# Performance work log

Measured on AMD Instinct MI355X. Metric: run time of the kernel, lower is better.

## Reference

```python
import jax, jax.numpy as jnp
import numpy as np

MAX_LANES = 5
DELTA_V = 1.0
DELTA_D = 6.0


def setup_inputs() -> dict:
    key = jax.random.key(0)
    k1, k2 = jax.random.split(key)
    targets = jax.random.randint(k1, (32, 360, 640), 0, 6, dtype=jnp.int32)
    embedding_vector = jax.random.normal(k2, (32, 4, 360, 640), dtype=jnp.float32)
    return {"targets": targets, "embedding_vector": embedding_vector}


def reference(targets, embedding_vector):
    B, C, H, W = embedding_vector.shape
    L = MAX_LANES
    P = H * W
    t = targets.reshape(B, P)                      # [B,P] labels 0..L
    e = embedding_vector.reshape(B, C, P)          # [B,C,P]

    # per-(batch, lane) segment counts and means
    onehot = (t[:, None, :] == jnp.arange(1, L + 1, dtype=t.dtype)[None, :, None])  # [B,L,P]
    counts = onehot.sum(-1)                        # [B,L] int
    valid = counts > 1                             # lane used only if >1 points
    sums = jnp.einsum('blp,bcp->blc', onehot.astype(e.dtype), e)   # [B,L,C]
    means = sums / jnp.maximum(counts, 1)[..., None].astype(e.dtype)  # [B,L,C]

    # ---- variance (pull) loss: per-point distance to its lane mean ----
    means_ext = jnp.concatenate([jnp.zeros((B, 1, C), e.dtype), means], axis=1)  # [B,L+1,C]
    mean_pix = jnp.take_along_axis(means_ext, t[..., None].astype(jnp.int32), axis=1)  # [B,P,C]
    diff = e.transpose(0, 2, 1) - mean_pix         # [B,P,C]
    sq = jnp.sum(diff * diff, axis=-1)             # [B,P]
    dist = jnp.sqrt(jnp.maximum(sq, 1e-12))
    valid_ext = jnp.concatenate([jnp.zeros((B, 1), bool), valid], axis=1)  # [B,L+1]
    pix_valid = jnp.take_along_axis(valid_ext, t.astype(jnp.int32), axis=1)  # [B,P]
    hinge = jax.nn.relu(dist - DELTA_V)
    dist_sum = jnp.sum(jnp.where(pix_valid, hinge * hinge, 0.0))
    point_count = jnp.sum(jnp.where(valid, counts, 0)).astype(e.dtype)
    dist_loss = jnp.where(point_count > 0, dist_sum / jnp.maximum(point_count, 1.0), 0.0)

    # ---- distance (push) loss: pdist over valid lane means per batch ----
    d = means[:, :, None, :] - means[:, None, :, :]          # [B,L,L,C]
    psq = jnp.sum(d * d, axis=-1)                            # [B,L,L]
    pd = jnp.sqrt(jnp.maximum(psq, 1e-12))
    iu = jnp.arange(L)
    pair_mask = valid[:, :, None] & valid[:, None, :] & (iu[:, None] < iu[None, :])  # [B,L,L]
    ph = jax.nn.relu(DELTA_D - pd)
    per_batch_sum = jnp.sum(jnp.where(pair_mask, ph * ph, 0.0), axis=(1, 2))  # [B]
    npairs = pair_mask.sum((1, 2)).astype(e.dtype)           # [B]
    batch_has = npairs > 0                                   # needs >=2 valid lanes
    var_b = jnp.where(batch_has, per_batch_sum / jnp.maximum(npairs, 1.0), 0.0)
    n_batches = batch_has.sum().astype(e.dtype)
    var_loss = jnp.where(n_batches > 0, var_b.sum() / jnp.maximum(n_batches, 1.0), 0.0)

    return dist_loss + var_loss
```

## Files before the change

kernel.cpp:

```cpp
#include <hip/hip_runtime.h>
#include <math.h>

#define B 32
#define C 4
#define P (360*640)
#define L 5
#define DELTA_V 1.0f
#define DELTA_D 6.0f

#define BLKX 45
#define ITER1 5
#define NBLK3 (B*BLKX)
#define PSTRIDE 48

__device__ __forceinline__ float waveReduce(float v) {
#pragma unroll
    for (int off = 32; off; off >>= 1) v += __shfl_down(v, off, 64);
    return v;
}

__global__ __launch_bounds__(256, 4) void seg_sums_k(const int* __restrict__ tgt,
                                                     const float* __restrict__ emb,
                                                     float* __restrict__ partial,
                                                     unsigned char* __restrict__ tpk) {
    const int x = blockIdx.x, c = blockIdx.y, b = blockIdx.z;
    const int tid = threadIdx.x;

    const int4*   t4 = (const int4*)(tgt + (size_t)b * P);
    const float4* ec = (const float4*)(emb + ((size_t)b * C + c) * P);

    int4   tv[ITER1];
    float4 ev[ITER1];
#pragma unroll
    for (int it = 0; it < ITER1; ++it) {
        const int g = (x + it * BLKX) * 256 + tid;
        tv[it] = t4[g];
        ev[it] = ec[g];
    }

    if (c == 0) {
        uchar4* tp4 = (uchar4*)(tpk + (size_t)b * P);
#pragma unroll
        for (int it = 0; it < ITER1; ++it) {
            const int g = (x + it * BLKX) * 256 + tid;
            tp4[g] = make_uchar4((unsigned char)tv[it].x, (unsigned char)tv[it].y,
                                 (unsigned char)tv[it].z, (unsigned char)tv[it].w);
        }
    }

    float s[L], n[L];
#pragma unroll
    for (int l = 0; l < L; ++l) { s[l] = 0.f; n[l] = 0.f; }

    auto acc1 = [&](int tt, float e) {
#pragma unroll
        for (int l = 0; l < L; ++l) {
            float m = (tt == l + 1) ? 1.0f : 0.0f;
            n[l] += m;
            s[l] = fmaf(m, e, s[l]);
        }
    };
#pragma unroll
    for (int it = 0; it < ITER1; ++it) {
        acc1(tv[it].x, ev[it].x);
        acc1(tv[it].y, ev[it].y);
        acc1(tv[it].z, ev[it].z);
        acc1(tv[it].w, ev[it].w);
    }

    float vals[2*L];
#pragma unroll
    for (int l = 0; l < L; ++l) { vals[l] = s[l]; vals[L + l] = n[l]; }

    __shared__ float red[4][2*L];
    const int lane = tid & 63, wave = tid >> 6;
#pragma unroll
    for (int k = 0; k < 2*L; ++k) {
        float r = waveReduce(vals[k]);
        if (lane == 0) red[wave][k] = r;
    }
    __syncthreads();
    if (tid < L) {
        const float r = red[0][tid] + red[1][tid] + red[2][tid] + red[3][tid];
        partial[((size_t)b * 25 + c * L + tid) * PSTRIDE + x] = r;
    } else if (c == 0 && tid < 2*L) {
        const float r = red[0][tid] + red[1][tid] + red[2][tid] + red[3][tid];
        partial[((size_t)b * 25 + 20 + (tid - L)) * PSTRIDE + x] = r;
    }
}

__global__ __launch_bounds__(256, 4) void pull_k(const unsigned char* __restrict__ tpk,
                                                 const float* __restrict__ emb,
                                                 const float* __restrict__ partial,
                                                 float* __restrict__ meansG,
                                                 float* __restrict__ validG,
                                                 float* __restrict__ cntvG,
                                                 float* __restrict__ pullp) {
    __shared__ float  praw[25];
    __shared__ float4 lmean[L + 1];
    __shared__ float  lvalid[L + 1];
    __shared__ float  lred[4];
    const int xb = blockIdx.x, b = blockIdx.y;
    const int tid = threadIdx.x;
    const int lane = tid & 63, wave = tid >> 6;

    for (int v = wave; v < 25; v += 4) {
        float pv = (lane < BLKX) ? partial[((size_t)b * 25 + v) * PSTRIDE + lane] : 0.f;
        pv = waveReduce(pv);
        if (lane == 0) praw[v] = pv;
    }
    __syncthreads();
    if (tid < L) {
        const float cnt = praw[20 + tid];
        const bool  vld = cnt > 1.5f;
        const float inv = 1.0f / fmaxf(cnt, 1.0f);
        float4 m = make_float4(praw[tid] * inv, praw[5 + tid] * inv,
                               praw[10 + tid] * inv, praw[15 + tid] * inv);
        lmean[tid + 1]  = m;
        lvalid[tid + 1] = vld ? 1.f : 0.f;
        if (xb == 0) {
            *(float4*)(meansG + ((size_t)b * L + tid) * 4) = m;
            validG[b * L + tid] = vld ? 1.f : 0.f;
            cntvG[b * L + tid]  = vld ? cnt : 0.f;
        }
    }
    if (tid == 8) { lmean[0] = make_float4(0.f, 0.f, 0.f, 0.f); lvalid[0] = 0.f; }
    __syncthreads();

    const uchar4* tp4 = (const uchar4*)(tpk + (size_t)b * P);
    const float4* e0  = (const float4*)(emb + ((size_t)b * C + 0) * P);
    const float4* e1  = (const float4*)(emb + ((size_t)b * C + 1) * P);
    const float4* e2  = (const float4*)(emb + ((size_t)b * C + 2) * P);
    const float4* e3  = (const float4*)(emb + ((size_t)b * C + 3) * P);

    float acc = 0.f;
    auto proc1 = [&](int tt, float v0, float v1, float v2, float v3) {
        float4 m = lmean[tt];
        float d0 = v0 - m.x, d1 = v1 - m.y, d2 = v2 - m.z, d3 = v3 - m.w;
        float sq   = d0*d0 + d1*d1 + d2*d2 + d3*d3;
        float dist = sqrtf(fmaxf(sq, 1e-12f));
        float h    = fmaxf(dist - DELTA_V, 0.f);
        acc = fmaf(lvalid[tt] * h, h, acc);
    };
    auto consume = [&](uchar4 t, const float4& a0, const float4& a1,
                       const float4& a2, const float4& a3) {
        proc1(t.x, a0.x, a1.x, a2.x, a3.x);
        proc1(t.y, a0.y, a1.y, a2.y, a3.y);
        proc1(t.z, a0.z, a1.z, a2.z, a3.z);
        proc1(t.w, a0.w, a1.w, a2.w, a3.w);
    };

    {
        const int g0 = xb * 256 + tid, g1 = (xb + BLKX) * 256 + tid;
        uchar4 t0 = tp4[g0], t1 = tp4[g1];
        float4 a0 = e0[g0], a1 = e1[g0], a2 = e2[g0], a3 = e3[g0];
        float4 b0 = e0[g1], b1 = e1[g1], b2 = e2[g1], b3 = e3[g1];
        consume(t0, a0, a1, a2, a3);
        consume(t1, b0, b1, b2, b3);
    }
    {
        const int g0 = (xb + 2*BLKX) * 256 + tid, g1 = (xb + 3*BLKX) * 256 + tid;
        uchar4 t0 = tp4[g0], t1 = tp4[g1];
        float4 a0 = e0[g0], a1 = e1[g0], a2 = e2[g0], a3 = e3[g0];
        float4 b0 = e0[g1], b1 = e1[g1], b2 = e2[g1], b3 = e3[g1];
        consume(t0, a0, a1, a2, a3);
        consume(t1, b0, b1, b2, b3);
    }
    {
        const int g0 = (xb + 4*BLKX) * 256 + tid;
        uchar4 t0 = tp4[g0];
        float4 a0 = e0[g0], a1 = e1[g0], a2 = e2[g0], a3 = e3[g0];
        consume(t0, a0, a1, a2, a3);
    }

    float r = waveReduce(acc);
    if (lane == 0) lred[wave] = r;
    __syncthreads();
    if (tid == 0)
        pullp[b * BLKX + xb] = lred[0] + lred[1] + lred[2] + lred[3];
}

__global__ __launch_bounds__(256) void finish_k(const float* __restrict__ pullp,
                                                const float* __restrict__ meansG,
                                                const float* __restrict__ validG,
                                                const float* __restrict__ cntvG,
                                                float* __restrict__ out) {
    __shared__ float red[4][4];
    const int tid = threadIdx.x;
    const int lane = tid & 63, wave = tid >> 6;

    float vb = 0.f, has = 0.f;
    if (tid < B) {
        const float* mb = meansG + tid * L * 4;
        const float* vv = validG + tid * L;
        float ssum = 0.f, np = 0.f;
#pragma unroll
        for (int i = 0; i < L; ++i)
#pragma unroll
            for (int j = i + 1; j < L; ++j) {
                float ok = vv[i] * vv[j];
                float d0 = mb[i*4+0] - mb[j*4+0];
                float d1 = mb[i*4+1] - mb[j*4+1];
                float d2 = mb[i*4+2] - mb[j*4+2];
                float d3 = mb[i*4+3] - mb[j*4+3];
                float psq = d0*d0 + d1*d1 + d2*d2 + d3*d3;
                float pd  = sqrtf(fmaxf(psq, 1e-12f));
                float ph  = fmaxf(DELTA_D - pd, 0.f);
                ssum += ok * ph * ph;
                np   += ok;
            }
        if (np > 0.f) { vb = ssum / np; has = 1.f; }
    }
    float pc = (tid < B*L) ? cntvG[tid] : 0.f;
    float ps = 0.f;
    for (int i = tid; i < NBLK3; i += 256) ps += pullp[i];

    float rvb = waveReduce(vb);
    float rhs = waveReduce(has);
    float rpc = waveReduce(pc);
    float rps = waveReduce(ps);
    if (lane == 0) { red[wave][0]=rvb; red[wave][1]=rhs; red[wave][2]=rpc; red[wave][3]=rps; }
    __syncthreads();
    if (tid == 0) {
        float svb = red[0][0]+red[1][0]+red[2][0]+red[3][0];
        float shs = red[0][1]+red[1][1]+red[2][1]+red[3][1];
        float spc = red[0][2]+red[1][2]+red[2][2]+red[3][2];
        float sps = red[0][3]+red[1][3]+red[2][3]+red[3][3];
        float var = (shs > 0.f) ? svb / shs : 0.f;
        float dl  = (spc > 0.f) ? sps / fmaxf(spc, 1.f) : 0.f;
        out[0] = dl + var;
    }
}

extern "C" void kernel_launch(void* const* d_in, const int* in_sizes, int n_in,
                              void* d_out, int out_size, void* d_ws, size_t ws_size,
                              hipStream_t stream) {
    const int*   tgt = (const int*)d_in[0];
    const float* emb = (const float*)d_in[1];

    unsigned char* tpk = (unsigned char*)d_ws;
    float* fbase   = (float*)((char*)d_ws + (size_t)B * P);
    float* partial = fbase;
    float* meansG  = partial + (size_t)B * 25 * PSTRIDE;
    float* validG  = meansG + (size_t)B * L * 4;
    float* cntvG   = validG + B * L;
    float* pullp   = cntvG + B * L;

    seg_sums_k<<<dim3(BLKX, C, B), 256, 0, stream>>>(tgt, emb, partial, tpk);
    pull_k<<<dim3(BLKX, B), 256, 0, stream>>>(tpk, emb, partial,
                                              meansG, validG, cntvG, pullp);
    finish_k<<<1, 256, 0, stream>>>(pullp, meansG, validG, cntvG, (float*)d_out);
}
```

Baseline: 216.9 us.

## Process two channels per segment-sum block and fuse finish into pull kernel

The segment-sum kernel now accumulates two embedding channels per block, so each target tile is loaded twice instead of four times, reducing global read traffic. The final reduction kernel is merged into the pull kernel using an atomic counter and a last-block-done pattern, removing one launch. This adds more registers per thread and a global atomic plus fences at the end of each pull block.

```diff
diff --git a/kernel.cpp b/kernel.cpp
--- a/kernel.cpp
+++ b/kernel.cpp
@@ -9,7 +9,6 @@
 #define DELTA_D 6.0f
 
 #define BLKX 45
-#define ITER1 5
 #define NBLK3 (B*BLKX)
 #define PSTRIDE 48
 
@@ -22,70 +21,93 @@
 __global__ __launch_bounds__(256, 4) void seg_sums_k(const int* __restrict__ tgt,
                                                      const float* __restrict__ emb,
                                                      float* __restrict__ partial,
-                                                     unsigned char* __restrict__ tpk) {
-    const int x = blockIdx.x, c = blockIdx.y, b = blockIdx.z;
+                                                     unsigned char* __restrict__ tpk,
+                                                     unsigned int* __restrict__ counter) {
+    const int x = blockIdx.x, cp = blockIdx.y, b = blockIdx.z;
     const int tid = threadIdx.x;
-
+    if (x == 0 && cp == 0 && b == 0 && tid == 0) *counter = 0u;
+
+    const int c0 = 2 * cp;
     const int4*   t4 = (const int4*)(tgt + (size_t)b * P);
-    const float4* ec = (const float4*)(emb + ((size_t)b * C + c) * P);
-
-    int4   tv[ITER1];
-    float4 ev[ITER1];
-#pragma unroll
-    for (int it = 0; it < ITER1; ++it) {
-        const int g = (x + it * BLKX) * 256 + tid;
-        tv[it] = t4[g];
-        ev[it] = ec[g];
-    }
-
-    if (c == 0) {
-        uchar4* tp4 = (uchar4*)(tpk + (size_t)b * P);
-#pragma unroll
-        for (int it = 0; it < ITER1; ++it) {
-            const int g = (x + it * BLKX) * 256 + tid;
-            tp4[g] = make_uchar4((unsigned char)tv[it].x, (unsigned char)tv[it].y,
-                                 (unsigned char)tv[it].z, (unsigned char)tv[it].w);
-        }
-    }
-
-    float s[L], n[L];
-#pragma unroll
-    for (int l = 0; l < L; ++l) { s[l] = 0.f; n[l] = 0.f; }
-
-    auto acc1 = [&](int tt, float e) {
+    const float4* ea = (const float4*)(emb + ((size_t)b * C + c0    ) * P);
+    const float4* eb = (const float4*)(emb + ((size_t)b * C + c0 + 1) * P);
+    uchar4*      tp4 = (uchar4*)(tpk + (size_t)b * P);
+
+    float s0[L], s1[L], n[L];
+#pragma unroll
+    for (int l = 0; l < L; ++l) { s0[l] = 0.f; s1[l] = 0.f; n[l] = 0.f; }
+
+    auto acc1 = [&](int tt, float xa, float xb) {
 #pragma unroll
         for (int l = 0; l < L; ++l) {
             float m = (tt == l + 1) ? 1.0f : 0.0f;
-            n[l] += m;
-            s[l] = fmaf(m, e, s[l]);
-        }
-    };
-#pragma unroll
-    for (int it = 0; it < ITER1; ++it) {
-        acc1(tv[it].x, ev[it].x);
-        acc1(tv[it].y, ev[it].y);
-        acc1(tv[it].z, ev[it].z);
-        acc1(tv[it].w, ev[it].w);
-    }
-
-    float vals[2*L];
-#pragma unroll
-    for (int l = 0; l < L; ++l) { vals[l] = s[l]; vals[L + l] = n[l]; }
-
-    __shared__ float red[4][2*L];
+            n[l]  += m;
+            s0[l]  = fmaf(m, xa, s0[l]);
+            s1[l]  = fmaf(m, xb, s1[l]);
+        }
+    };
+    auto consume = [&](const int4& t, const float4& va, const float4& vb) {
+        acc1(t.x, va.x, vb.x);
+        acc1(t.y, va.y, vb.y);
+        acc1(t.z, va.z, vb.z);
+        acc1(t.w, va.w, vb.w);
+    };
+
+    {
+        const int g0 = x * 256 + tid, g1 = (x + BLKX) * 256 + tid;
+        int4   t0 = t4[g0], t1 = t4[g1];
+        float4 a0 = ea[g0], b0 = eb[g0], a1 = ea[g1], b1 = eb[g1];
+        if (cp == 0) {
+            tp4[g0] = make_uchar4((unsigned char)t0.x, (unsigned char)t0.y,
+                                  (unsigned char)t0.z, (unsigned char)t0.w);
+            tp4[g1] = make_uchar4((unsigned char)t1.x, (unsigned char)t1.y,
+                                  (unsigned char)t1.z, (unsigned char)t1.w);
+        }
+        consume(t0, a0, b0);
+        consume(t1, a1, b1);
+    }
+    {
+        const int g0 = (x + 2*BLKX) * 256 + tid, g1 = (x + 3*BLKX) * 256 + tid;
+        int4   t0 = t4[g0], t1 = t4[g1];
+        float4 a0 = ea[g0], b0 = eb[g0], a1 = ea[g1], b1 = eb[g1];
+        if (cp == 0) {
+            tp4[g0] = make_uchar4((unsigned char)t0.x, (unsigned char)t0.y,
+                                  (unsigned char)t0.z, (unsigned char)t0.w);
+            tp4[g1] = make_uchar4((unsigned char)t1.x, (unsigned char)t1.y,
+                                  (unsigned char)t1.z, (unsigned char)t1.w);
+        }
+        consume(t0, a0, b0);
+        consume(t1, a1, b1);
+    }
+    {
+        const int g0 = (x + 4*BLKX) * 256 + tid;
+        int4   t0 = t4[g0];
+        float4 a0 = ea[g0], b0 = eb[g0];
+        if (cp == 0)
+            tp4[g0] = make_uchar4((unsigned char)t0.x, (unsigned char)t0.y,
+                                  (unsigned char)t0.z, (unsigned char)t0.w);
+        consume(t0, a0, b0);
+    }
+
+    float vals[15];
+#pragma unroll
+    for (int l = 0; l < L; ++l) { vals[l] = s0[l]; vals[L + l] = s1[l]; vals[10 + l] = n[l]; }
+
+    __shared__ float red[4][15];
     const int lane = tid & 63, wave = tid >> 6;
 #pragma unroll
-    for (int k = 0; k < 2*L; ++k) {
+    for (int k = 0; k < 15; ++k) {
         float r = waveReduce(vals[k]);
         if (lane == 0) red[wave][k] = r;
     }
     __syncthreads();
-    if (tid < L) {
+    if (tid < 15) {
         const float r = red[0][tid] + red[1][tid] + red[2][tid] + red[3][tid];
-        partial[((size_t)b * 25 + c * L + tid) * PSTRIDE + x] = r;
-    } else if (c == 0 && tid < 2*L) {
-        const float r = red[0][tid] + red[1][tid] + red[2][tid] + red[3][tid];
-        partial[((size_t)b * 25 + 20 + (tid - L)) * PSTRIDE + x] = r;
+        int v;
+        if (cp == 0) v = (tid < 10) ? tid : (10 + tid);
+        else         v = (tid < 10) ? (10 + tid) : -1;
+        if (v >= 0)
+            partial[((size_t)b * 25 + v) * PSTRIDE + x] = r;
     }
 }
 
@@ -95,11 +117,14 @@
                                                  float* __restrict__ meansG,
                                                  float* __restrict__ validG,
                                                  float* __restrict__ cntvG,
-                                                 float* __restrict__ pullp) {
+                                                 float* __restrict__ pullp,
+                                                 unsigned int* __restrict__ counter,
+                                                 float* __restrict__ out) {
     __shared__ float  praw[25];
     __shared__ float4 lmean[L + 1];
     __shared__ float  lvalid[L + 1];
     __shared__ float  lred[4];
+    __shared__ int    sLast;
     const int xb = blockIdx.x, b = blockIdx.y;
     const int tid = threadIdx.x;
     const int lane = tid & 63, wave = tid >> 6;
@@ -176,18 +201,17 @@
     float r = waveReduce(acc);
     if (lane == 0) lred[wave] = r;
     __syncthreads();
-    if (tid == 0)
+    if (tid == 0) {
         pullp[b * BLKX + xb] = lred[0] + lred[1] + lred[2] + lred[3];
-}
-
-__global__ __launch_bounds__(256) void finish_k(const float* __restrict__ pullp,
-                                                const float* __restrict__ meansG,
-                                                const float* __restrict__ validG,
-                                                const float* __restrict__ cntvG,
-                                                float* __restrict__ out) {
-    __shared__ float red[4][4];
-    const int tid = threadIdx.x;
-    const int lane = tid & 63, wave = tid >> 6;
+        __threadfence();
+        unsigned int old = atomicAdd(counter, 1u);
+        sLast = (old == (unsigned int)(NBLK3 - 1)) ? 1 : 0;
+    }
+    __syncthreads();
+    if (!sLast) return;
+
+    __threadfence();
+    __shared__ float red2[4][4];
 
     float vb = 0.f, has = 0.f;
     if (tid < B) {
@@ -219,13 +243,13 @@
     float rhs = waveReduce(has);
     float rpc = waveReduce(pc);
     float rps = waveReduce(ps);
-    if (lane == 0) { red[wave][0]=rvb; red[wave][1]=rhs; red[wave][2]=rpc; red[wave][3]=rps; }
+    if (lane == 0) { red2[wave][0]=rvb; red2[wave][1]=rhs; red2[wave][2]=rpc; red2[wave][3]=rps; }
     __syncthreads();
     if (tid == 0) {
-        float svb = red[0][0]+red[1][0]+red[2][0]+red[3][0];
-        float shs = red[0][1]+red[1][1]+red[2][1]+red[3][1];
-        float spc = red[0][2]+red[1][2]+red[2][2]+red[3][2];
-        float sps = red[0][3]+red[1][3]+red[2][3]+red[3][3];
+        float svb = red2[0][0]+red2[1][0]+red2[2][0]+red2[3][0];
+        float shs = red2[0][1]+red2[1][1]+red2[2][1]+red2[3][1];
+        float spc = red2[0][2]+red2[1][2]+red2[2][2]+red2[3][2];
+        float sps = red2[0][3]+red2[1][3]+red2[2][3]+red2[3][3];
         float var = (shs > 0.f) ? svb / shs : 0.f;
         float dl  = (spc > 0.f) ? sps / fmaxf(spc, 1.f) : 0.f;
         out[0] = dl + var;
@@ -245,9 +269,9 @@
     float* validG  = meansG + (size_t)B * L * 4;
     float* cntvG   = validG + B * L;
     float* pullp   = cntvG + B * L;
-
-    seg_sums_k<<<dim3(BLKX, C, B), 256, 0, stream>>>(tgt, emb, partial, tpk);
-    pull_k<<<dim3(BLKX, B), 256, 0, stream>>>(tpk, emb, partial,
-                                              meansG, validG, cntvG, pullp);
-    finish_k<<<1, 256, 0, stream>>>(pullp, meansG, validG, cntvG, (float*)d_out);
-}
+    unsigned int* counter = (unsigned int*)(pullp + NBLK3);
+
+    seg_sums_k<<<dim3(BLKX, 2, B), 256, 0, stream>>>(tgt, emb, partial, tpk, counter);
+    pull_k<<<dim3(BLKX, B), 256, 0, stream>>>(tpk, emb, partial, meansG, validG,
+                                              cntvG, pullp, counter, (float*)d_out);
+}
```

Result: slower. 300.4 us (+38.5%).

## Pack labels in a separate pass and fold finish into pull via last-block counter

Applied to the files above, without the earlier changes.

Adds a pack kernel that reads the int32 labels once, writes the uint8 packed copy, and computes the per-lane counts. The segment-sum kernel then reads the 1-byte labels instead of rereading int32 labels for each of the 4 channels, which cuts label traffic. The finish kernel is merged into the pull kernel: an atomic counter picks the last block, which does the final reduction, saving one launch. The cost is an extra launch for the pack kernel and a serial dependency between pack and seg-sum.

```diff
diff --git a/kernel.cpp b/kernel.cpp
--- a/kernel.cpp
+++ b/kernel.cpp
@@ -19,44 +19,82 @@
     return v;
 }
 
-__global__ __launch_bounds__(256, 4) void seg_sums_k(const int* __restrict__ tgt,
+__global__ __launch_bounds__(256) void pack_k(const int* __restrict__ tgt,
+                                              unsigned char* __restrict__ tpk,
+                                              float* __restrict__ partial,
+                                              unsigned int* __restrict__ counter) {
+    const int x = blockIdx.x, b = blockIdx.y;
+    const int tid = threadIdx.x;
+    if (x == 0 && b == 0 && tid == 0) *counter = 0u;
+
+    const int4* t4  = (const int4*)(tgt + (size_t)b * P);
+    uchar4*     tp4 = (uchar4*)(tpk + (size_t)b * P);
+
+    int4 tv[ITER1];
+#pragma unroll
+    for (int it = 0; it < ITER1; ++it)
+        tv[it] = t4[(x + it * BLKX) * 256 + tid];
+
+#pragma unroll
+    for (int it = 0; it < ITER1; ++it)
+        tp4[(x + it * BLKX) * 256 + tid] =
+            make_uchar4((unsigned char)tv[it].x, (unsigned char)tv[it].y,
+                        (unsigned char)tv[it].z, (unsigned char)tv[it].w);
+
+    float n[L];
+#pragma unroll
+    for (int l = 0; l < L; ++l) n[l] = 0.f;
+#pragma unroll
+    for (int it = 0; it < ITER1; ++it) {
+#pragma unroll
+        for (int l = 0; l < L; ++l) {
+            n[l] += (tv[it].x == l + 1) ? 1.f : 0.f;
+            n[l] += (tv[it].y == l + 1) ? 1.f : 0.f;
+            n[l] += (tv[it].z == l + 1) ? 1.f : 0.f;
+            n[l] += (tv[it].w == l + 1) ? 1.f : 0.f;
+        }
+    }
+
+    __shared__ float red[4][L];
+    const int lane = tid & 63, wave = tid >> 6;
+#pragma unroll
+    for (int k = 0; k < L; ++k) {
+        float r = waveReduce(n[k]);
+        if (lane == 0) red[wave][k] = r;
+    }
+    __syncthreads();
+    if (tid < L) {
+        const float r = red[0][tid] + red[1][tid] + red[2][tid] + red[3][tid];
+        partial[((size_t)b * 25 + 20 + tid) * PSTRIDE + x] = r;
+    }
+}
+
+__global__ __launch_bounds__(256, 4) void seg_sums_k(const unsigned char* __restrict__ tpk,
                                                      const float* __restrict__ emb,
-                                                     float* __restrict__ partial,
-                                                     unsigned char* __restrict__ tpk) {
+                                                     float* __restrict__ partial) {
     const int x = blockIdx.x, c = blockIdx.y, b = blockIdx.z;
     const int tid = threadIdx.x;
 
-    const int4*   t4 = (const int4*)(tgt + (size_t)b * P);
-    const float4* ec = (const float4*)(emb + ((size_t)b * C + c) * P);
-
-    int4   tv[ITER1];
+    const uchar4* tp4 = (const uchar4*)(tpk + (size_t)b * P);
+    const float4* ec  = (const float4*)(emb + ((size_t)b * C + c) * P);
+
+    uchar4 tv[ITER1];
     float4 ev[ITER1];
 #pragma unroll
     for (int it = 0; it < ITER1; ++it) {
         const int g = (x + it * BLKX) * 256 + tid;
-        tv[it] = t4[g];
+        tv[it] = tp4[g];
         ev[it] = ec[g];
     }
 
-    if (c == 0) {
-        uchar4* tp4 = (uchar4*)(tpk + (size_t)b * P);
-#pragma unroll
-        for (int it = 0; it < ITER1; ++it) {
-            const int g = (x + it * BLKX) * 256 + tid;
-            tp4[g] = make_uchar4((unsigned char)tv[it].x, (unsigned char)tv[it].y,
-                                 (unsigned char)tv[it].z, (unsigned char)tv[it].w);
-        }
-    }
-
-    float s[L], n[L];
-#pragma unroll
-    for (int l = 0; l < L; ++l) { s[l] = 0.f; n[l] = 0.f; }
+    float s[L];
+#pragma unroll
+    for (int l = 0; l < L; ++l) s[l] = 0.f;
 
     auto acc1 = [&](int tt, float e) {
 #pragma unroll
         for (int l = 0; l < L; ++l) {
             float m = (tt == l + 1) ? 1.0f : 0.0f;
-            n[l] += m;
             s[l] = fmaf(m, e, s[l]);
         }
     };
@@ -68,24 +106,17 @@
         acc1(tv[it].w, ev[it].w);
     }
 
-    float vals[2*L];
-#pragma unroll
-    for (int l = 0; l < L; ++l) { vals[l] = s[l]; vals[L + l] = n[l]; }
-
-    __shared__ float red[4][2*L];
+    __shared__ float red[4][L];
     const int lane = tid & 63, wave = tid >> 6;
 #pragma unroll
-    for (int k = 0; k < 2*L; ++k) {
-        float r = waveReduce(vals[k]);
+    for (int k = 0; k < L; ++k) {
+        float r = waveReduce(s[k]);
         if (lane == 0) red[wave][k] = r;
     }
     __syncthreads();
     if (tid < L) {
         const float r = red[0][tid] + red[1][tid] + red[2][tid] + red[3][tid];
         partial[((size_t)b * 25 + c * L + tid) * PSTRIDE + x] = r;
-    } else if (c == 0 && tid < 2*L) {
-        const float r = red[0][tid] + red[1][tid] + red[2][tid] + red[3][tid];
-        partial[((size_t)b * 25 + 20 + (tid - L)) * PSTRIDE + x] = r;
     }
 }
 
@@ -95,11 +126,14 @@
                                                  float* __restrict__ meansG,
                                                  float* __restrict__ validG,
                                                  float* __restrict__ cntvG,
-                                                 float* __restrict__ pullp) {
+                                                 float* __restrict__ pullp,
+                                                 unsigned int* __restrict__ counter,
+                                                 float* __restrict__ out) {
     __shared__ float  praw[25];
     __shared__ float4 lmean[L + 1];
     __shared__ float  lvalid[L + 1];
     __shared__ float  lred[4];
+    __shared__ int    sLast;
     const int xb = blockIdx.x, b = blockIdx.y;
     const int tid = threadIdx.x;
     const int lane = tid & 63, wave = tid >> 6;
@@ -176,18 +210,17 @@
     float r = waveReduce(acc);
     if (lane == 0) lred[wave] = r;
     __syncthreads();
-    if (tid == 0)
+    if (tid == 0) {
         pullp[b * BLKX + xb] = lred[0] + lred[1] + lred[2] + lred[3];
-}
-
-__global__ __launch_bounds__(256) void finish_k(const float* __restrict__ pullp,
-                                                const float* __restrict__ meansG,
-                                                const float* __restrict__ validG,
-                                                const float* __restrict__ cntvG,
-                                                float* __restrict__ out) {
-    __shared__ float red[4][4];
-    const int tid = threadIdx.x;
-    const int lane = tid & 63, wave = tid >> 6;
+        __threadfence();
+        unsigned int old = atomicAdd(counter, 1u);
+        sLast = (old == (unsigned int)(NBLK3 - 1)) ? 1 : 0;
+    }
+    __syncthreads();
+    if (!sLast) return;
+
+    __threadfence();
+    __shared__ float red2[4][4];
 
     float vb = 0.f, has = 0.f;
     if (tid < B) {
@@ -219,13 +252,13 @@
     float rhs = waveReduce(has);
     float rpc = waveReduce(pc);
     float rps = waveReduce(ps);
-    if (lane == 0) { red[wave][0]=rvb; red[wave][1]=rhs; red[wave][2]=rpc; red[wave][3]=rps; }
+    if (lane == 0) { red2[wave][0]=rvb; red2[wave][1]=rhs; red2[wave][2]=rpc; red2[wave][3]=rps; }
     __syncthreads();
     if (tid == 0) {
-        float svb = red[0][0]+red[1][0]+red[2][0]+red[3][0];
-        float shs = red[0][1]+red[1][1]+red[2][1]+red[3][1];
-        float spc = red[0][2]+red[1][2]+red[2][2]+red[3][2];
-        float sps = red[0][3]+red[1][3]+red[2][3]+red[3][3];
+        float svb = red2[0][0]+red2[1][0]+red2[2][0]+red2[3][0];
+        float shs = red2[0][1]+red2[1][1]+red2[2][1]+red2[3][1];
+        float spc = red2[0][2]+red2[1][2]+red2[2][2]+red2[3][2];
+        float sps = red2[0][3]+red2[1][3]+red2[2][3]+red2[3][3];
         float var = (shs > 0.f) ? svb / shs : 0.f;
         float dl  = (spc > 0.f) ? sps / fmaxf(spc, 1.f) : 0.f;
         out[0] = dl + var;
@@ -245,9 +278,10 @@
     float* validG  = meansG + (size_t)B * L * 4;
     float* cntvG   = validG + B * L;
     float* pullp   = cntvG + B * L;
-
-    seg_sums_k<<<dim3(BLKX, C, B), 256, 0, stream>>>(tgt, emb, partial, tpk);
-    pull_k<<<dim3(BLKX, B), 256, 0, stream>>>(tpk, emb, partial,
-                                              meansG, validG, cntvG, pullp);
-    finish_k<<<1, 256, 0, stream>>>(pullp, meansG, validG, cntvG, (float*)d_out);
-}
+    unsigned int* counter = (unsigned int*)(pullp + NBLK3);
+
+    pack_k<<<dim3(BLKX, B), 256, 0, stream>>>(tgt, tpk, partial, counter);
+    seg_sums_k<<<dim3(BLKX, C, B), 256, 0, stream>>>(tpk, emb, partial);
+    pull_k<<<dim3(BLKX, B), 256, 0, stream>>>(tpk, emb, partial, meansG, validG,
+                                              cntvG, pullp, counter, (float*)d_out);
+}
```

Measured after the change: 260.6 us. 1.2x slower.
